# Optimization experiments

Measured on AMD Instinct MI355X. Metric: run time of the kernel, lower is better.

## Reference

```python
import jax, jax.numpy as jnp
import numpy as np

B, M, C_IN, H, W = 8, 64, 2048, 16, 16
IMG = 512          # image size in pixels (feature stride 32)
OUT = 7            # ROIAlign output size
SCALE = 1.0 / 32.0
SR = 2             # samples per bin; equals ceil(roi_extent/7) for the generated boxes (sampling_ratio=0 behavior)
C2 = C_IN // 2     # 1024
D_ROI, D_BOX = 1024, 256
D_PAIR = 2 * (D_ROI + D_BOX)   # 2560
D_G = D_PAIR // 2              # 1280


def setup_inputs() -> dict:
    key = jax.random.key(0)
    ks = jax.random.split(key, 12)
    s = 0.02
    im_feat = jax.random.normal(ks[0], (B, C_IN, H, W), jnp.float32)
    # XYXY boxes; sizes in (230,440)px so scaled roi extent is in (7,14] -> adaptive sampling ratio == 2
    xy1 = jax.random.uniform(ks[1], (B, M, 2), jnp.float32, 0.0, 60.0)
    wh = jax.random.uniform(ks[2], (B, M, 2), jnp.float32, 230.0, 440.0)
    boxes = jnp.concatenate([xy1, xy1 + wh], -1)
    normalized_boxes = boxes / IMG
    params = dict(
        proj_w=jax.random.normal(ks[3], (C2, C_IN), jnp.float32) * s, proj_b=jnp.zeros((C2,), jnp.float32),
        conv_w=jax.random.normal(ks[4], (256, C2, 3, 3), jnp.float32) * s, conv_b=jnp.zeros((256,), jnp.float32),
        bn_g=jnp.ones((256,), jnp.float32), bn_b=jnp.zeros((256,), jnp.float32),
        bn_m=jnp.zeros((256,), jnp.float32), bn_v=jnp.ones((256,), jnp.float32),
        fc_w=jax.random.normal(ks[5], (D_ROI, 256 * OUT * OUT), jnp.float32) * s, fc_b=jnp.zeros((D_ROI,), jnp.float32),
        ln1_g=jnp.ones((D_ROI,), jnp.float32), ln1_b=jnp.zeros((D_ROI,), jnp.float32),
        box_w=jax.random.normal(ks[6], (D_BOX, 4), jnp.float32) * s, box_b=jnp.zeros((D_BOX,), jnp.float32),
        ln2_g=jnp.ones((D_BOX,), jnp.float32), ln2_b=jnp.zeros((D_BOX,), jnp.float32),
        g1_w=jax.random.normal(ks[7], (D_G, D_PAIR), jnp.float32) * s, g1_b=jnp.zeros((D_G,), jnp.float32),
        g2_w=jax.random.normal(ks[8], (D_G, D_G), jnp.float32) * s, g2_b=jnp.zeros((D_G,), jnp.float32),
        g3_w=jax.random.normal(ks[9], (D_G, D_G), jnp.float32) * s, g3_b=jnp.zeros((D_G,), jnp.float32),
    )
    return dict(im_feat=im_feat, boxes=boxes, normalized_boxes=normalized_boxes, **params)


def _layer_norm(x, g, b, eps=1e-5):
    mu = x.mean(-1, keepdims=True)
    var = ((x - mu) ** 2).mean(-1, keepdims=True)
    return (x - mu) * jax.lax.rsqrt(var + eps) * g + b


def _roi_align(feat, rois, bidx):
    # feat [B,C,Hf,Wf]; rois [N,4] XYXY image coords; bidx [N] int. ROIAlignV2 (aligned=True), 2x2 samples/bin.
    Hf, Wf = feat.shape[2], feat.shape[3]
    x1 = rois[:, 0] * SCALE - 0.5
    y1 = rois[:, 1] * SCALE - 0.5
    bw = (rois[:, 2] - rois[:, 0]) * SCALE / OUT
    bh = (rois[:, 3] - rois[:, 1]) * SCALE / OUT
    ii = (jnp.arange(OUT * SR, dtype=jnp.float32) + 0.5) / SR  # sample offsets in bin units
    xs = x1[:, None] + bw[:, None] * ii[None, :]               # [N, OUT*SR]
    ys = y1[:, None] + bh[:, None] * ii[None, :]

    def interp1(v, size):
        valid = (v >= -1.0) & (v <= size)
        v = jnp.clip(v, 0.0, None)
        lo = jnp.floor(v).astype(jnp.int32)
        over = lo >= size - 1
        lo = jnp.where(over, size - 1, lo)
        v = jnp.where(over, lo.astype(v.dtype), v)
        hi = jnp.where(over, lo, lo + 1)
        return lo, hi, v - lo, valid

    def bilin(b, ys_, xs_):
        img = feat[b]  # [C,Hf,Wf]
        yl, yh, wy, vy = interp1(ys_, Hf)
        xl, xh, wx, vx = interp1(xs_, Wf)
        g = lambda yi, xi: img[:, yi][:, :, xi]  # [C,S,S]
        val = (g(yl, xl) * (1 - wy)[None, :, None] * (1 - wx)[None, None, :]
               + g(yl, xh) * (1 - wy)[None, :, None] * wx[None, None, :]
               + g(yh, xl) * wy[None, :, None] * (1 - wx)[None, None, :]
               + g(yh, xh) * wy[None, :, None] * wx[None, None, :])
        mask = (vy[:, None] & vx[None, :]).astype(val.dtype)
        return val * mask

    vals = jax.vmap(bilin)(bidx, ys, xs)  # [N,C,OUT*SR,OUT*SR]
    N, C = vals.shape[0], vals.shape[1]
    return vals.reshape(N, C, OUT, SR, OUT, SR).mean((3, 5))  # avg over samples per bin


def reference(im_feat, boxes, normalized_boxes, proj_w, proj_b, conv_w, conv_b, bn_g, bn_b, bn_m, bn_v,
              fc_w, fc_b, ln1_g, ln1_b, box_w, box_b, ln2_g, ln2_b, g1_w, g1_b, g2_w, g2_b, g3_w, g3_b):
    # 1x1 conv projection
    x = jnp.einsum('bchw,oc->bohw', im_feat, proj_w) + proj_b[None, :, None, None]
    rois = boxes.reshape(B * M, 4)
    bidx = jnp.repeat(jnp.arange(B), M)
    r = _roi_align(x, rois, bidx)  # [BM, C2, 7, 7]
    # roi_processor: conv3x3 -> BN(eval) -> ReLU -> flatten -> Linear -> ReLU
    r = jax.lax.conv_general_dilated(r, conv_w, (1, 1), 'SAME',
                                     dimension_numbers=('NCHW', 'OIHW', 'NCHW')) + conv_b[None, :, None, None]
    r = (r - bn_m[None, :, None, None]) * jax.lax.rsqrt(bn_v + 1e-5)[None, :, None, None] \
        * bn_g[None, :, None, None] + bn_b[None, :, None, None]
    r = jax.nn.relu(r)
    r = jax.nn.relu(r.reshape(B * M, -1) @ fc_w.T + fc_b)
    r = _layer_norm(r, ln1_g, ln1_b)                       # [BM, 1024]
    nb = normalized_boxes.reshape(B * M, 4) * 2.0 - 1.0
    bf = _layer_norm(nb @ box_w.T + box_b, ln2_g, ln2_b)   # [BM, 256]
    feats = jnp.concatenate([r, bf], -1).reshape(B, M, D_ROI + D_BOX)

    def rel(xm):  # relation network over one image's M rois
        xi = jnp.broadcast_to(xm[None, :, :], (M, M, D_ROI + D_BOX))  # xi[a,b]=x[b]
        xj = jnp.broadcast_to(xm[:, None, :], (M, M, D_ROI + D_BOX))  # xj[a,b]=x[a]
        p = jnp.concatenate([xi, xj], -1).reshape(M * M, D_PAIR)
        h = jax.nn.relu(p @ g1_w.T + g1_b)
        h = jax.nn.relu(h @ g2_w.T + g2_b)
        h = jax.nn.relu(h @ g3_w.T + g3_b)
        return h.sum(0)

    return jax.vmap(rel)(feats)  # [B, 1280]
```

## Files before the change

### kernel.cpp

```cpp
#include <hip/hip_runtime.h>
#include <hip/hip_bf16.h>

typedef __attribute__((ext_vector_type(8))) short short8;
typedef __attribute__((ext_vector_type(4))) float floatx4;
typedef unsigned short u16;

#define GLDS16(gp, lp) __builtin_amdgcn_global_load_lds(                        \
    (const __attribute__((address_space(1))) void*)(gp),                        \
    (__attribute__((address_space(3))) void*)(lp), 16, 0, 0)

__device__ inline u16 f2bf(float f) {
    unsigned u = __float_as_uint(f);
    unsigned r = (u + 0x7fffu + ((u >> 16) & 1u)) >> 16;
    return (u16)r;
}

__device__ inline void block_reduce2(float& s, float& ss) {
    #pragma unroll
    for (int o = 32; o > 0; o >>= 1) {
        s  += __shfl_down(s, o);
        ss += __shfl_down(ss, o);
    }
    __shared__ float red[8];
    const int t = threadIdx.x;
    if ((t & 63) == 0) { red[t >> 6] = s; red[4 + (t >> 6)] = ss; }
    __syncthreads();
    s  = red[0] + red[1] + red[2] + red[3];
    ss = red[4] + red[5] + red[6] + red[7];
}

template<int AMODE, int EPI, int CMODE>
__global__ __launch_bounds__(256)
void gemm_bf16(const u16* __restrict__ A, const u16* __restrict__ B,
               const float* __restrict__ P1, const float* __restrict__ P2,
               void* __restrict__ Cv,
               int M, int N, int Kc, int lda, int ldb, int ldc)
{
    __shared__ short As[3][4096];
    __shared__ short Bs[3][4096];

    const int t  = threadIdx.x;
    const int w  = t >> 6, l = t & 63;
    const int wr = w >> 1, wc = w & 1;
    const int l16 = l & 15, lr = l >> 4;

    const int nwg = gridDim.x * gridDim.y;
    const int bid = blockIdx.y * gridDim.x + blockIdx.x;
    const int cpx = nwg >> 3;
    const int sw  = (bid & 7) * cpx + (bid >> 3);
    const int n0 = (sw % gridDim.x) * 128;
    const int m0 = (sw / gridDim.x) * 128;
    const int kbase = blockIdx.z * Kc;

    const int srow  = w * 16 + (l >> 2);
    const int skoff = (((l & 3) ^ ((l >> 2) & 3)) * 8);

    const u16* aRow0 = nullptr; const u16* aRow1 = nullptr;
    size_t aSp0 = 0, aSp1 = 0;
    if (AMODE == 0) {
        aRow0 = A + (size_t)(m0 + srow) * lda + kbase + skoff;
        aRow1 = A + (size_t)(m0 + 64 + srow) * lda + kbase + skoff;
    } else {
        const int r0 = m0 + srow, r1 = r0 + 64;
        const int roi0 = r0 / 49, sp0 = r0 - roi0 * 49;
        const int roi1 = r1 / 49, sp1 = r1 - roi1 * 49;
        aSp0 = ((size_t)roi0 * 81 + (sp0 / 7) * 9 + (sp0 % 7)) * 1024 + skoff;
        aSp1 = ((size_t)roi1 * 81 + (sp1 / 7) * 9 + (sp1 % 7)) * 1024 + skoff;
    }
    const u16* bRow0 = B + (size_t)(n0 + srow) * ldb + kbase + skoff;
    const u16* bRow1 = B + (size_t)(n0 + 64 + srow) * ldb + kbase + skoff;

    auto stage = [&](int buf, int k0) {
        if (AMODE == 0) {
            GLDS16(aRow0 + k0, As[buf] + w * 512);
            GLDS16(aRow1 + k0, As[buf] + 2048 + w * 512);
        } else {
            const int kk  = kbase + k0;
            const int tap = kk >> 10;
            const size_t off = (size_t)((tap / 3) * 9 + (tap % 3)) * 1024 + (kk & 1023);
            GLDS16(A + aSp0 + off, As[buf] + w * 512);
            GLDS16(A + aSp1 + off, As[buf] + 2048 + w * 512);
        }
        GLDS16(bRow0 + k0, Bs[buf] + w * 512);
        GLDS16(bRow1 + k0, Bs[buf] + 2048 + w * 512);
    };

    floatx4 acc[4][4] = {};

    auto compute = [&](int buf) {
        const short* as = As[buf];
        const short* bs = Bs[buf];
        short8 af[4], bfr[4];
        #pragma unroll
        for (int i = 0; i < 4; ++i) {
            const int row = wr * 64 + i * 16 + l16;
            af[i] = *reinterpret_cast<const short8*>(&as[row * 32 + ((lr ^ (row & 3)) * 8)]);
        }
        #pragma unroll
        for (int j = 0; j < 4; ++j) {
            const int row = wc * 64 + j * 16 + l16;
            bfr[j] = *reinterpret_cast<const short8*>(&bs[row * 32 + ((lr ^ (row & 3)) * 8)]);
        }
        __builtin_amdgcn_s_setprio(1);
        #pragma unroll
        for (int i = 0; i < 4; ++i)
            #pragma unroll
            for (int j = 0; j < 4; ++j)
                acc[i][j] = __builtin_amdgcn_mfma_f32_16x16x32_bf16(af[i], bfr[j], acc[i][j], 0, 0, 0);
        __builtin_amdgcn_s_setprio(0);
    };

    const int nsteps = Kc >> 5;

    stage(0, 0); stage(1, 32); stage(2, 64);

    for (int i = 0; i < nsteps - 2; ++i) {
        asm volatile("s_waitcnt vmcnt(8)" ::: "memory");
        __builtin_amdgcn_s_barrier();
        __builtin_amdgcn_sched_barrier(0);
        compute(i % 3);
        __builtin_amdgcn_sched_barrier(0);
        __builtin_amdgcn_s_barrier();
        __builtin_amdgcn_sched_barrier(0);
        if (i < nsteps - 3) stage(i % 3, (i + 3) * 32);
    }
    {
        const int i = nsteps - 2;
        asm volatile("s_waitcnt vmcnt(4)" ::: "memory");
        __builtin_amdgcn_s_barrier();
        __builtin_amdgcn_sched_barrier(0);
        compute(i % 3);
    }
    {
        const int i = nsteps - 1;
        asm volatile("s_waitcnt vmcnt(0)" ::: "memory");
        __builtin_amdgcn_s_barrier();
        __builtin_amdgcn_sched_barrier(0);
        compute(i % 3);
    }

    const int mBase = m0 + wr * 64;
    const int nBase = n0 + wc * 64;

    if (CMODE == 2) {
        __shared__ float red2[2][128];
        float csum[4];
        #pragma unroll
        for (int j = 0; j < 4; ++j) {
            const int n = nBase + j * 16 + l16;
            const float b1 = P1[n];
            float s = 0.f;
            #pragma unroll
            for (int i = 0; i < 4; ++i)
                #pragma unroll
                for (int r = 0; r < 4; ++r)
                    s += fmaxf(acc[i][j][r] + b1, 0.f);
            s += __shfl_xor(s, 16);
            s += __shfl_xor(s, 32);
            csum[j] = s;
        }
        __syncthreads();
        if (l < 16) {
            #pragma unroll
            for (int j = 0; j < 4; ++j)
                red2[wr][wc * 64 + j * 16 + l16] = csum[j];
        }
        __syncthreads();
        float* C = (float*)Cv + (size_t)(m0 >> 12) * ldc;
        if (t < 128) atomicAdd(&C[n0 + t], red2[0][t] + red2[1][t]);
        return;
    }

    #pragma unroll
    for (int i = 0; i < 4; ++i) {
        #pragma unroll
        for (int j = 0; j < 4; ++j) {
            const int n = nBase + j * 16 + l16;
            const float b1 = (EPI >= 1) ? P1[n] : 0.f;
            const float b2 = (EPI == 3) ? P2[n] : 0.f;
            #pragma unroll
            for (int r = 0; r < 4; ++r) {
                float v = acc[i][j][r];
                if (EPI == 1)      v += b1;
                else if (EPI == 2) v = fmaxf(v + b1, 0.f);
                else if (EPI == 3) v = fmaxf(v * b1 + b2, 0.f);
                const int m = mBase + i * 16 + lr * 4 + r;
                if (CMODE == 0)      ((float*)Cv)[(size_t)m * ldc + n] = v;
                else if (CMODE == 4) ((u16*)Cv)[(size_t)m * ldc + n] = f2bf(v);
                else if (CMODE == 3) atomicAdd(&((float*)Cv)[(size_t)m * ldc + n], v);
                else if (CMODE == 1) {
                    const int roi = m / 49, sp = m - roi * 49;
                    ((u16*)Cv)[(size_t)roi * 12544 + n * 49 + sp] = f2bf(v);
                }
            }
        }
    }
}

__global__ __launch_bounds__(256)
void transpose_proj(const float* __restrict__ in, u16* __restrict__ out)
{
    __shared__ float tile[64][65];
    const int b = blockIdx.z;
    const int c0 = blockIdx.y * 64;
    const int h0 = blockIdx.x * 64;
    const int t = threadIdx.x;
    const float* src = in + ((size_t)b * 2048 + c0) * 256 + h0;
    #pragma unroll
    for (int p = 0; p < 16; ++p) {
        const int idx = p * 256 + t;
        const int r = idx >> 6, c = idx & 63;
        tile[r][c] = src[(size_t)r * 256 + c];
    }
    __syncthreads();
    u16* dst = out + ((size_t)b * 256 + h0) * 2048 + c0;
    #pragma unroll
    for (int p = 0; p < 16; ++p) {
        const int idx = p * 256 + t;
        const int r = idx >> 6, c = idx & 63;
        dst[(size_t)r * 2048 + c] = f2bf(tile[c][r]);
    }
}

__global__ __launch_bounds__(256)
void zero_halo(u16* __restrict__ r_pad)
{
    const int blk = blockIdx.x;
    const int roi = blk >> 5, h = blk & 31;
    int p;
    if (h < 9)       p = h;
    else if (h < 18) p = 72 + (h - 9);
    else { const int r = (h - 18) >> 1, s = (h - 18) & 1; p = (r + 1) * 9 + s * 8; }
    uint2* o = reinterpret_cast<uint2*>(r_pad + ((size_t)roi * 81 + p) * 1024);
    o[threadIdx.x] = make_uint2(0u, 0u);
}

__global__ __launch_bounds__(256)
void roialign_kernel(const float* __restrict__ x_cl, const float* __restrict__ boxes,
                     u16* __restrict__ r_pad)
{
    const int blk = blockIdx.x;
    const int n = blk / 49, bin = blk % 49;
    const int py = bin / 7, px = bin % 7;
    const int b = n >> 6;
    const float* roi = boxes + n * 4;
    const float x1 = roi[0] * (1.f/32.f) - 0.5f;
    const float y1 = roi[1] * (1.f/32.f) - 0.5f;
    const float bw = (roi[2] - roi[0]) * (1.f/32.f) * (1.0f / 7.0f);
    const float bh = (roi[3] - roi[1]) * (1.f/32.f) * (1.0f / 7.0f);
    const int t = threadIdx.x;

    float acc[4] = {0.f, 0.f, 0.f, 0.f};
    #pragma unroll
    for (int sy = 0; sy < 2; ++sy) {
        #pragma unroll
        for (int sx = 0; sx < 2; ++sx) {
            const float yv = y1 + bh * ((float)(py * 2 + sy) + 0.5f) * 0.5f;
            const float xv = x1 + bw * ((float)(px * 2 + sx) + 0.5f) * 0.5f;
            const bool vy = (yv >= -1.0f) && (yv <= 16.0f);
            const bool vx = (xv >= -1.0f) && (xv <= 16.0f);
            if (!(vy && vx)) continue;
            float yc = fmaxf(yv, 0.f);
            int yl = (int)floorf(yc);
            int yh; if (yl >= 15) { yl = 15; yc = 15.f; yh = 15; } else yh = yl + 1;
            const float wy = yc - (float)yl;
            float xc = fmaxf(xv, 0.f);
            int xl = (int)floorf(xc);
            int xh; if (xl >= 15) { xl = 15; xc = 15.f; xh = 15; } else xh = xl + 1;
            const float wx = xc - (float)xl;

            const float w00 = (1.f - wy) * (1.f - wx), w01 = (1.f - wy) * wx;
            const float w10 = wy * (1.f - wx),         w11 = wy * wx;
            const float* p00 = x_cl + ((size_t)b * 256 + yl * 16 + xl) * 1024;
            const float* p01 = x_cl + ((size_t)b * 256 + yl * 16 + xh) * 1024;
            const float* p10 = x_cl + ((size_t)b * 256 + yh * 16 + xl) * 1024;
            const float* p11 = x_cl + ((size_t)b * 256 + yh * 16 + xh) * 1024;
            #pragma unroll
            for (int cc = 0; cc < 4; ++cc) {
                const int c = t + cc * 256;
                acc[cc] += w00 * p00[c] + w01 * p01[c] + w10 * p10[c] + w11 * p11[c];
            }
        }
    }
    u16* o = r_pad + ((size_t)n * 81 + (py + 1) * 9 + (px + 1)) * 1024;
    #pragma unroll
    for (int cc = 0; cc < 4; ++cc) o[t + cc * 256] = f2bf(acc[cc] * 0.25f);
}

__global__ __launch_bounds__(256)
void pack_conv(const float* __restrict__ conv_w, const float* __restrict__ conv_b,
               const float* __restrict__ bn_g, const float* __restrict__ bn_b,
               const float* __restrict__ bn_m, const float* __restrict__ bn_v,
               u16* __restrict__ wpack, float* __restrict__ scale, float* __restrict__ shift)
{
    const long idx = (long)blockIdx.x * 256 + threadIdx.x;
    if (idx < 2359296L) {
        const int oc = (int)(idx / 9216), k = (int)(idx % 9216);
        const int tap = k >> 10, ic = k & 1023;
        wpack[idx] = f2bf(conv_w[(long)oc * 9216 + ic * 9 + tap]);
    }
    if (idx < 256) {
        const float s = bn_g[idx] * rsqrtf(bn_v[idx] + 1e-5f);
        scale[idx] = s;
        shift[idx] = (conv_b[idx] - bn_m[idx]) * s + bn_b[idx];
    }
}

__global__ __launch_bounds__(256)
void cvt_bf16(const float* __restrict__ in, u16* __restrict__ out, int n4)
{
    const int i = blockIdx.x * 256 + threadIdx.x;
    if (i < n4) {
        const float4 v = reinterpret_cast<const float4*>(in)[i];
        ushort4 o; o.x = f2bf(v.x); o.y = f2bf(v.y); o.z = f2bf(v.z); o.w = f2bf(v.w);
        reinterpret_cast<ushort4*>(out)[i] = o;
    }
}

__global__ __launch_bounds__(256)
void pack_g1(const float* __restrict__ g1w, u16* __restrict__ out)
{
    const int j = blockIdx.x * 256 + threadIdx.x;
    if (j >= 2560 * 320) return;
    const int np = j / 320, k4 = (j - np * 320) * 4;
    const int srow = (np < 1280) ? np : np - 1280;
    const int soff = (np < 1280) ? 0 : 1280;
    const float4 v = *reinterpret_cast<const float4*>(&g1w[(size_t)srow * 2560 + soff + k4]);
    ushort4 o; o.x = f2bf(v.x); o.y = f2bf(v.y); o.z = f2bf(v.z); o.w = f2bf(v.w);
    *reinterpret_cast<ushort4*>(&out[(size_t)np * 1280 + k4]) = o;
}

__global__ __launch_bounds__(256)
void ln1_kernel(const float* __restrict__ in, const float* __restrict__ fb,
                const float* __restrict__ g, const float* __restrict__ b,
                u16* __restrict__ feats)
{
    const int n = blockIdx.x, t = threadIdx.x;
    float4 v = *reinterpret_cast<const float4*>(in + (size_t)n * 1024 + t * 4);
    const float4 bb = *reinterpret_cast<const float4*>(fb + t * 4);
    v.x = fmaxf(v.x + bb.x, 0.f); v.y = fmaxf(v.y + bb.y, 0.f);
    v.z = fmaxf(v.z + bb.z, 0.f); v.w = fmaxf(v.w + bb.w, 0.f);
    float s  = v.x + v.y + v.z + v.w;
    float ss = v.x*v.x + v.y*v.y + v.z*v.z + v.w*v.w;
    block_reduce2(s, ss);
    const float mu  = s * (1.f / 1024.f);
    const float var = ss * (1.f / 1024.f) - mu * mu;
    const float r   = rsqrtf(var + 1e-5f);
    const float4 gp = *reinterpret_cast<const float4*>(g + t * 4);
    const float4 bp = *reinterpret_cast<const float4*>(b + t * 4);
    ushort4 o;
    o.x = f2bf((v.x - mu) * r * gp.x + bp.x);
    o.y = f2bf((v.y - mu) * r * gp.y + bp.y);
    o.z = f2bf((v.z - mu) * r * gp.z + bp.z);
    o.w = f2bf((v.w - mu) * r * gp.w + bp.w);
    *reinterpret_cast<ushort4*>(feats + (size_t)n * 1280 + t * 4) = o;
}

__global__ __launch_bounds__(256)
void box_kernel(const float* __restrict__ nb, const float* __restrict__ bw,
                const float* __restrict__ bb, const float* __restrict__ g,
                const float* __restrict__ be, u16* __restrict__ feats)
{
    const int n = blockIdx.x, j = threadIdx.x;
    const float4 q = *reinterpret_cast<const float4*>(nb + n * 4);
    const float4 w = *reinterpret_cast<const float4*>(bw + j * 4);
    const float v = (q.x * 2.f - 1.f) * w.x + (q.y * 2.f - 1.f) * w.y
                  + (q.z * 2.f - 1.f) * w.z + (q.w * 2.f - 1.f) * w.w + bb[j];
    float s = v, ss = v * v;
    block_reduce2(s, ss);
    const float mu  = s * (1.f / 256.f);
    const float var = ss * (1.f / 256.f) - mu * mu;
    feats[(size_t)n * 1280 + 1024 + j] = f2bf((v - mu) * rsqrtf(var + 1e-5f) * g[j] + be[j]);
}

__global__ __launch_bounds__(256)
void pair_kernel(const float* __restrict__ UV, const float* __restrict__ g1b,
                 u16* __restrict__ h1, int imgbase)
{
    const int pidx = blockIdx.y;
    const int img = imgbase + (pidx >> 12);
    const int a = (pidx >> 6) & 63, b = pidx & 63;
    const int col = blockIdx.x * 256 + threadIdx.x;
    const float v = UV[(size_t)(img * 64 + b) * 2560 + col]
                  + UV[(size_t)(img * 64 + a) * 2560 + 1280 + col] + g1b[col];
    h1[(size_t)pidx * 1280 + col] = f2bf(fmaxf(v, 0.f));
}

__global__ void zero_f32(float* __restrict__ p, int n) {
    const int i = blockIdx.x * 256 + threadIdx.x;
    if (i < n) p[i] = 0.f;
}

extern "C" void kernel_launch(void* const* d_in, const int* in_sizes, int n_in,
                              void* d_out, int out_size, void* d_ws, size_t ws_size,
                              hipStream_t stream)
{
    const float* im_feat = (const float*)d_in[0];
    const float* boxes   = (const float*)d_in[1];
    const float* nboxes  = (const float*)d_in[2];
    const float* proj_w  = (const float*)d_in[3];
    const float* proj_b  = (const float*)d_in[4];
    const float* conv_w  = (const float*)d_in[5];
    const float* conv_b  = (const float*)d_in[6];
    const float* bn_g    = (const float*)d_in[7];
    const float* bn_b    = (const float*)d_in[8];
    const float* bn_m    = (const float*)d_in[9];
    const float* bn_v    = (const float*)d_in[10];
    const float* fc_w    = (const float*)d_in[11];
    const float* fc_b    = (const float*)d_in[12];
    const float* ln1_g   = (const float*)d_in[13];
    const float* ln1_b   = (const float*)d_in[14];
    const float* box_w   = (const float*)d_in[15];
    const float* box_b   = (const float*)d_in[16];
    const float* ln2_g   = (const float*)d_in[17];
    const float* ln2_b   = (const float*)d_in[18];
    const float* g1_w    = (const float*)d_in[19];
    const float* g1_b    = (const float*)d_in[20];
    const float* g2_w    = (const float*)d_in[21];
    const float* g2_b    = (const float*)d_in[22];
    const float* g3_w    = (const float*)d_in[23];
    const float* g3_b    = (const float*)d_in[24];
    float* out = (float*)d_out;
    (void)in_sizes; (void)n_in; (void)out_size; (void)ws_size;

    char* base = (char*)d_ws;
    size_t o = 0;
    auto carve = [&](size_t bytes) { char* p = base + o; o += (bytes + 15) & ~(size_t)15; return p; };
    float* x_cl    = (float*)carve(8388608);
    u16*   imT     = (u16*)  carve(8388608);
    u16*   convout = (u16*)  carve(12845056);
    float* fc_out  = (float*)carve(2097152);
    u16*   feats   = (u16*)  carve(1310720);
    float* UV      = (float*)carve(5242880);
    u16*   wpack   = (u16*)  carve(4718592);
    float* scale   = (float*)carve(1024);
    float* shift   = (float*)carve(1024);
    u16*   projwb  = (u16*)  carve(4194304);
    u16*   fcwb    = (u16*)  carve(25690112);
    u16*   g1wb    = (u16*)  carve(6553600);
    u16*   g2wb    = (u16*)  carve(3276800);
    u16*   g3wb    = (u16*)  carve(3276800);
    char*  big     = carve(84934656);
    u16*   r_pad   = (u16*)big;
    u16*   h1      = (u16*)big;
    u16*   h2      = (u16*)(big + 41943040);

    zero_f32<<<40, 256, 0, stream>>>(out, 10240);
    zero_f32<<<2048, 256, 0, stream>>>(fc_out, 524288);
    zero_f32<<<5120, 256, 0, stream>>>(UV, 1310720);

    cvt_bf16<<<2048, 256, 0, stream>>>(proj_w, projwb, 524288);
    cvt_bf16<<<12544, 256, 0, stream>>>(fc_w, fcwb, 3211264);
    cvt_bf16<<<1600, 256, 0, stream>>>(g2_w, g2wb, 409600);
    cvt_bf16<<<1600, 256, 0, stream>>>(g3_w, g3wb, 409600);
    pack_g1<<<3200, 256, 0, stream>>>(g1_w, g1wb);
    pack_conv<<<9216, 256, 0, stream>>>(conv_w, conv_b, bn_g, bn_b, bn_m, bn_v, wpack, scale, shift);

    transpose_proj<<<dim3(4, 32, 8), 256, 0, stream>>>(im_feat, imT);
    gemm_bf16<0, 1, 0><<<dim3(8, 16, 1), 256, 0, stream>>>(
        imT, projwb, proj_b, nullptr, x_cl, 2048, 1024, 2048, 2048, 2048, 1024);

    zero_halo<<<16384, 256, 0, stream>>>(r_pad);
    roialign_kernel<<<25088, 256, 0, stream>>>(x_cl, boxes, r_pad);

    gemm_bf16<2, 3, 1><<<dim3(2, 196, 1), 256, 0, stream>>>(
        r_pad, wpack, scale, shift, convout, 25088, 256, 9216, 0, 9216, 0);

    gemm_bf16<0, 0, 3><<<dim3(8, 4, 4), 256, 0, stream>>>(
        convout, fcwb, nullptr, nullptr, fc_out, 512, 1024, 3136, 12544, 12544, 1024);

    ln1_kernel<<<512, 256, 0, stream>>>(fc_out, fc_b, ln1_g, ln1_b, feats);
    box_kernel<<<512, 256, 0, stream>>>(nboxes, box_w, box_b, ln2_g, ln2_b, feats);

    gemm_bf16<0, 0, 3><<<dim3(20, 4, 2), 256, 0, stream>>>(
        feats, g1wb, nullptr, nullptr, UV, 512, 2560, 640, 1280, 1280, 2560);

    for (int h = 0; h < 2; ++h) {
        pair_kernel<<<dim3(5, 16384), 256, 0, stream>>>(UV, g1_b, h1, h * 4);
        gemm_bf16<0, 2, 4><<<dim3(10, 128, 1), 256, 0, stream>>>(
            h1, g2wb, g2_b, nullptr, h2, 16384, 1280, 1280, 1280, 1280, 1280);
        gemm_bf16<0, 2, 2><<<dim3(10, 128, 1), 256, 0, stream>>>(
            h2, g3wb, g3_b, nullptr, out + h * 4 * 1280, 16384, 1280, 1280, 1280, 1280, 1280);
    }
}
```

Baseline: 937.2 us.

## Add 256x256-tile 512-thread GEMM kernel for relation-network g2/g3 layers

Introduces a new bf16 MFMA GEMM with 256x256 output tiles, 8 waves per block, a 4-deep LDS ring filled by direct global-to-LDS loads, XOR-swizzled LDS layout and split A/B prefetch interleaved with MFMA issue under raised priority. It replaces the previous 128-ish-tile GEMM for the two large 16384x1280x1280 layers, aiming to raise arithmetic intensity per LDS/global byte. The fused bias+ReLU+column-sum epilogue with atomics is kept for the final layer. Larger tiles mean only 320 blocks, which leaves some tail imbalance across CUs, and the large register and LDS footprint limits occupancy.

```diff
diff --git a/kernel.cpp b/kernel.cpp
--- a/kernel.cpp
+++ b/kernel.cpp
@@ -27,6 +27,150 @@
     __syncthreads();
     s  = red[0] + red[1] + red[2] + red[3];
     ss = red[4] + red[5] + red[6] + red[7];
+}
+
+template<int EPI, int CMODE>
+__global__ __launch_bounds__(512, 2)
+void gemm256(const u16* __restrict__ A, const u16* __restrict__ B,
+             const float* __restrict__ P1, void* __restrict__ Cv,
+             int Kc, int lda, int ldb, int ldc)
+{
+    __shared__ short L[4][16384];
+    __shared__ float red2[2][256];
+
+    const int t = threadIdx.x;
+    const int w = t >> 6, l = t & 63;
+    const int wr = w >> 2, wc = w & 3;
+    const int l16 = l & 15, lr = l >> 4;
+
+    const int nwg = gridDim.x * gridDim.y;
+    const int bid = blockIdx.y * gridDim.x + blockIdx.x;
+    const int cpx = nwg >> 3;
+    const int sw  = (bid & 7) * cpx + (bid >> 3);
+    const int n0 = (sw % gridDim.x) * 256;
+    const int m0 = (sw / gridDim.x) * 256;
+
+    const int r0 = w * 16 + (l >> 2);
+    const int sl = l & 3;
+    const u16* aS[2]; const u16* bS[2];
+    #pragma unroll
+    for (int g = 0; g < 2; ++g) {
+        const int r  = g * 128 + r0;
+        const int ks = (sl ^ ((r >> 1) & 3)) * 8;
+        aS[g] = A + (size_t)(m0 + r) * lda + ks;
+        bS[g] = B + (size_t)(n0 + r) * ldb + ks;
+    }
+
+    auto stageA = [&](int tt) {
+        short* d = L[tt & 3];
+        GLDS16(aS[0] + tt * 32, d + w * 512);
+        GLDS16(aS[1] + tt * 32, d + 4096 + w * 512);
+    };
+    auto stageB = [&](int tt) {
+        short* d = L[tt & 3] + 8192;
+        GLDS16(bS[0] + tt * 32, d + w * 512);
+        GLDS16(bS[1] + tt * 32, d + 4096 + w * 512);
+    };
+
+    int aOff[8], bOff[4];
+    #pragma unroll
+    for (int m = 0; m < 8; ++m) {
+        const int row = wr * 128 + m * 16 + l16;
+        aOff[m] = row * 32 + ((lr ^ ((row >> 1) & 3)) * 8);
+    }
+    #pragma unroll
+    for (int n = 0; n < 4; ++n) {
+        const int row = wc * 64 + n * 16 + l16;
+        bOff[n] = 8192 + row * 32 + ((lr ^ ((row >> 1) & 3)) * 8);
+    }
+
+    floatx4 acc[8][4] = {};
+    const int nsteps = Kc >> 5;
+
+    stageA(0); stageB(0); stageA(1); stageB(1); stageA(2); stageB(2);
+
+    for (int tt = 0; tt < nsteps; ++tt) {
+        if (tt <= nsteps - 3)      asm volatile("s_waitcnt vmcnt(8)" ::: "memory");
+        else if (tt == nsteps - 2) asm volatile("s_waitcnt vmcnt(4)" ::: "memory");
+        else                       asm volatile("s_waitcnt vmcnt(0)" ::: "memory");
+        __builtin_amdgcn_s_barrier();
+        __builtin_amdgcn_sched_barrier(0);
+
+        const short* buf = L[tt & 3];
+        const bool pre = (tt + 3 < nsteps);
+        short8 af[4], bfr[4];
+
+        if (pre) stageA(tt + 3);
+        #pragma unroll
+        for (int n = 0; n < 4; ++n)
+            bfr[n] = *reinterpret_cast<const short8*>(&buf[bOff[n]]);
+        #pragma unroll
+        for (int m = 0; m < 4; ++m)
+            af[m] = *reinterpret_cast<const short8*>(&buf[aOff[m]]);
+        __builtin_amdgcn_s_setprio(1);
+        #pragma unroll
+        for (int m = 0; m < 4; ++m)
+            #pragma unroll
+            for (int n = 0; n < 4; ++n)
+                acc[m][n] = __builtin_amdgcn_mfma_f32_16x16x32_bf16(af[m], bfr[n], acc[m][n], 0, 0, 0);
+        __builtin_amdgcn_s_setprio(0);
+
+        if (pre) stageB(tt + 3);
+        #pragma unroll
+        for (int m = 0; m < 4; ++m)
+            af[m] = *reinterpret_cast<const short8*>(&buf[aOff[4 + m]]);
+        __builtin_amdgcn_s_setprio(1);
+        #pragma unroll
+        for (int m = 0; m < 4; ++m)
+            #pragma unroll
+            for (int n = 0; n < 4; ++n)
+                acc[4 + m][n] = __builtin_amdgcn_mfma_f32_16x16x32_bf16(af[m], bfr[n], acc[4 + m][n], 0, 0, 0);
+        __builtin_amdgcn_s_setprio(0);
+    }
+
+    if (CMODE == 2) {
+        float csum[4];
+        #pragma unroll
+        for (int n = 0; n < 4; ++n) {
+            const int col = n0 + wc * 64 + n * 16 + l16;
+            const float b1 = P1[col];
+            float s = 0.f;
+            #pragma unroll
+            for (int m = 0; m < 8; ++m)
+                #pragma unroll
+                for (int r = 0; r < 4; ++r)
+                    s += fmaxf(acc[m][n][r] + b1, 0.f);
+            s += __shfl_xor(s, 16);
+            s += __shfl_xor(s, 32);
+            csum[n] = s;
+        }
+        if (l < 16) {
+            #pragma unroll
+            for (int n = 0; n < 4; ++n)
+                red2[wr][wc * 64 + n * 16 + l16] = csum[n];
+        }
+        __syncthreads();
+        if (t < 256) {
+            float* C = (float*)Cv + (size_t)(m0 >> 12) * ldc;
+            atomicAdd(&C[n0 + t], red2[0][t] + red2[1][t]);
+        }
+        return;
+    }
+
+    u16* C = (u16*)Cv;
+    #pragma unroll
+    for (int m = 0; m < 8; ++m) {
+        #pragma unroll
+        for (int n = 0; n < 4; ++n) {
+            const int col = n0 + wc * 64 + n * 16 + l16;
+            const float b1 = P1[col];
+            #pragma unroll
+            for (int r = 0; r < 4; ++r) {
+                const int row = m0 + wr * 128 + m * 16 + lr * 4 + r;
+                C[(size_t)row * ldc + col] = f2bf(fmaxf(acc[m][n][r] + b1, 0.f));
+            }
+        }
+    }
 }
 
 template<int AMODE, int EPI, int CMODE>
@@ -477,9 +621,9 @@
 
     for (int h = 0; h < 2; ++h) {
         pair_kernel<<<dim3(5, 16384), 256, 0, stream>>>(UV, g1_b, h1, h * 4);
-        gemm_bf16<0, 2, 4><<<dim3(10, 128, 1), 256, 0, stream>>>(
-            h1, g2wb, g2_b, nullptr, h2, 16384, 1280, 1280, 1280, 1280, 1280);
-        gemm_bf16<0, 2, 2><<<dim3(10, 128, 1), 256, 0, stream>>>(
-            h2, g3wb, g3_b, nullptr, out + h * 4 * 1280, 16384, 1280, 1280, 1280, 1280, 1280);
-    }
-}
+        gemm256<2, 4><<<dim3(5, 64), 512, 0, stream>>>(
+            h1, g2wb, g2_b, h2, 1280, 1280, 1280, 1280);
+        gemm256<2, 2><<<dim3(5, 64), 512, 0, stream>>>(
+            h2, g3wb, g3_b, out + h * 4 * 1280, 1280, 1280, 1280, 1280);
+    }
+}
```

Result: slower. 990.5 us (+5.7%).
